# Kernel tuning notes

Hardware: AMD Instinct MI355X
Metric: run time of the kernel (lower is better)

## Reference

```python
import jax, jax.numpy as jnp
import numpy as np

B, S, D, H, FF = 8, 1024, 2048, 16, 8192
Dh = D // H
EPS = 1e-5

def _layernorm(x, g, b):
    m = jnp.mean(x, axis=-1, keepdims=True)
    v = jnp.mean(jnp.square(x - m), axis=-1, keepdims=True)
    return (x - m) / jnp.sqrt(v + EPS) * g + b

def setup_inputs() -> dict:
    key = jax.random.key(0)
    ks = jax.random.split(key, 12)
    sc_d = 1.0 / np.sqrt(D)
    sc_ff = 1.0 / np.sqrt(FF)
    return {
        "x": jax.random.normal(ks[0], (B, S, D), dtype=jnp.float32),
        "mask": jnp.ones((S, S), dtype=jnp.int32),
        "Wq": jax.random.normal(ks[1], (D, D), dtype=jnp.float32) * sc_d,
        "bq": jnp.zeros((D,), dtype=jnp.float32),
        "Wk": jax.random.normal(ks[2], (D, D), dtype=jnp.float32) * sc_d,
        "bk": jnp.zeros((D,), dtype=jnp.float32),
        "Wv": jax.random.normal(ks[3], (D, D), dtype=jnp.float32) * sc_d,
        "bv": jnp.zeros((D,), dtype=jnp.float32),
        "Wo": jax.random.normal(ks[4], (D, D), dtype=jnp.float32) * sc_d,
        "bo": jnp.zeros((D,), dtype=jnp.float32),
        "W1": jax.random.normal(ks[5], (FF, D), dtype=jnp.float32) * sc_d,
        "b1": jnp.zeros((FF,), dtype=jnp.float32),
        "W2": jax.random.normal(ks[6], (D, FF), dtype=jnp.float32) * sc_ff,
        "b2": jnp.zeros((D,), dtype=jnp.float32),
        "g1": jnp.ones((D,), dtype=jnp.float32),
        "be1": jnp.zeros((D,), dtype=jnp.float32),
        "g2": jnp.ones((D,), dtype=jnp.float32),
        "be2": jnp.zeros((D,), dtype=jnp.float32),
    }

def reference(x, mask, Wq, bq, Wk, bk, Wv, bv, Wo, bo, W1, b1, W2, b2, g1, be1, g2, be2):
    # --- multi-head attention (chunk along d_model == reshape to heads) ---
    q = (x @ Wq.T + bq).reshape(B, S, H, Dh)
    k = (x @ Wk.T + bk).reshape(B, S, H, Dh)
    v = (x @ Wv.T + bv).reshape(B, S, H, Dh)
    score = jnp.einsum('bqhd,bkhd->bhqk', q, k) / jnp.sqrt(jnp.float32(Dh))
    score = jnp.where(mask == 0, jnp.float32(-1e9), score)
    attn = jax.nn.softmax(score, axis=-1)
    out = jnp.einsum('bhqk,bkhd->bqhd', attn, v).reshape(B, S, D)
    attn_out = out @ Wo.T + bo
    # --- residual + post-LN ---
    x1 = _layernorm(attn_out + x, g1, be1)
    # --- FFN ---
    h = jax.nn.relu(x1 @ W1.T + b1)
    ffn_out = h @ W2.T + b2
    return _layernorm(ffn_out + x1, g2, be2)
```

## Files before the change

kernel.cpp:

```cpp
#include <hip/hip_runtime.h>
#include <cstdint>
#include <cstddef>


typedef unsigned short u16;
typedef unsigned int   u32;
typedef unsigned long long u64;
typedef __attribute__((ext_vector_type(8))) short short8;
typedef __attribute__((ext_vector_type(4))) float f32x4;

constexpr int Bc  = 8;
constexpr int Sc  = 1024;
constexpr int Dc  = 2048;
constexpr int Hc  = 16;
constexpr int Dhc = 128;
constexpr int FFc = 8192;
constexpr int Mc  = Bc * Sc;

__device__ __forceinline__ u16 f2b(float f) {
  u32 u = __builtin_bit_cast(u32, f);
  u += 0x7fffu + ((u >> 16) & 1u);
  return (u16)(u >> 16);
}
__device__ __forceinline__ u32 pack2(float a, float b) {
  return (u32)f2b(a) | ((u32)f2b(b) << 16);
}
__device__ __forceinline__ void unpack8(uint4 u, float* f) {
  u32 w[4] = {u.x, u.y, u.z, u.w};
#pragma unroll
  for (int i = 0; i < 4; ++i) {
    f[2 * i + 0] = __builtin_bit_cast(float, w[i] << 16);
    f[2 * i + 1] = __builtin_bit_cast(float, w[i] & 0xffff0000u);
  }
}

#define GLOAD_LDS16(gp, lp)                                                    \
  __builtin_amdgcn_global_load_lds(                                            \
      (const __attribute__((address_space(1))) void*)(gp),                     \
      (__attribute__((address_space(3))) void*)(lp), 16, 0, 0)

__global__ __launch_bounds__(256) void cvt_f32_bf16(const float* __restrict__ in,
                                                    u16* __restrict__ out, int n) {
  int i = (blockIdx.x * 256 + threadIdx.x) << 2;
  if (i >= n) return;
  float4 v = *(const float4*)(in + i);
  ushort4 o;
  o.x = f2b(v.x); o.y = f2b(v.y); o.z = f2b(v.z); o.w = f2b(v.w);
  *(ushort4*)(out + i) = o;
}

__global__ __launch_bounds__(256) void mask_bits(const int* __restrict__ mask,
                                                 u64* __restrict__ mb) {
  int t = blockIdx.x * 256 + threadIdx.x;
  int r = t >> 4, wd = t & 15;
  const int* p = mask + (size_t)r * Sc + wd * 64;
  u64 bits = 0;
#pragma unroll 16
  for (int i = 0; i < 64; i += 4) {
    int4 q = *(const int4*)(p + i);
    bits |= (u64)(q.x != 0) << (i + 0);
    bits |= (u64)(q.y != 0) << (i + 1);
    bits |= (u64)(q.z != 0) << (i + 2);
    bits |= (u64)(q.w != 0) << (i + 3);
  }
  mb[t] = bits;
}

template <int MODE>
__global__ __launch_bounds__(512, 2) void gemm256tb(const u16* __restrict__ A,
                                                    const u16* __restrict__ Bt,
                                                    const float* __restrict__ bias,
                                                    u16* __restrict__ C,
                                                    int M, int N, int K) {
  __shared__ u16 Abuf[4][256 * 32];
  __shared__ u16 Bbuf[4][256 * 32];

  const int nbn = N >> 8;
  const int nwg = (M >> 8) * nbn;
  int bid = blockIdx.x;
  int sw = (bid & 7) * (nwg >> 3) + (bid >> 3);
  const int m0 = (sw / nbn) << 8;
  const int n0 = (sw % nbn) << 8;

  const int tid  = threadIdx.x;
  const int lane = tid & 63;
  const int w    = tid >> 6;
  const int wm   = w >> 2;
  const int wn   = w & 3;

  const int rowA = lane & 15;
  const int g4   = lane >> 4;

  const int p16  = lane << 4;
  const int wsw  = p16 ^ (((p16 >> 9) & 1) << 5);
  const int s_rr = wsw >> 6;
  const int s_cc = (wsw & 63) >> 1;

  const int sb = (rowA * 64 + g4 * 16) ^ (((rowA >> 3) & 1) << 5);

  const int NT = K >> 5;

  const u16* Asrc = A  + (size_t)(m0 + w * 32 + s_rr) * K + s_cc;
  const u16* Bsrc = Bt + (size_t)(n0 + w * 32 + s_rr) * K + s_cc;

  auto stageA = [&](int buf, int tt) {
#pragma unroll
    for (int i = 0; i < 2; ++i)
      GLOAD_LDS16(Asrc + (size_t)i * 16 * K + tt * 32,
                  &Abuf[buf][(2 * w + i) * 512]);
  };
  auto stageB = [&](int buf, int tt) {
#pragma unroll
    for (int i = 0; i < 2; ++i)
      GLOAD_LDS16(Bsrc + (size_t)i * 16 * K + tt * 32,
                  &Bbuf[buf][(2 * w + i) * 512]);
  };

  f32x4 acc[8][4];
#pragma unroll
  for (int m = 0; m < 8; ++m)
#pragma unroll
    for (int n = 0; n < 4; ++n) acc[m][n] = (f32x4){0.f, 0.f, 0.f, 0.f};

  stageA(0, 0); stageB(0, 0);
  stageA(1, 1); stageB(1, 1);
  stageA(2, 2); stageB(2, 2);
  asm volatile("s_waitcnt vmcnt(8)" ::: "memory");
  __builtin_amdgcn_s_barrier();

  for (int t = 0; t < NT; ++t) {
    const int rd  = t & 3;
    const int wr_ = (t + 3) & 3;
    const bool st = (t + 3) < NT;

    short8 bF[4], aF[4];
#pragma unroll
    for (int n = 0; n < 4; ++n)
      bF[n] = *(const short8*)((const char*)&Bbuf[rd][(wn * 4 + n) * 512] + sb);
#pragma unroll
    for (int i = 0; i < 4; ++i)
      aF[i] = *(const short8*)((const char*)&Abuf[rd][(wm * 8 + i) * 512] + sb);
    if (st) stageA(wr_, t + 3);
    __builtin_amdgcn_s_barrier();
    asm volatile("s_waitcnt lgkmcnt(0)" ::: "memory");
    __builtin_amdgcn_sched_barrier(0);
    __builtin_amdgcn_s_setprio(1);
#pragma unroll
    for (int i = 0; i < 4; ++i)
#pragma unroll
      for (int n = 0; n < 4; ++n)
        acc[i][n] = __builtin_amdgcn_mfma_f32_16x16x32_bf16(aF[i], bF[n], acc[i][n], 0, 0, 0);
    __builtin_amdgcn_s_setprio(0);
    __builtin_amdgcn_s_barrier();

#pragma unroll
    for (int i = 0; i < 4; ++i)
      aF[i] = *(const short8*)((const char*)&Abuf[rd][(wm * 8 + 4 + i) * 512] + sb);
    if (st) stageB(wr_, t + 3);
    __builtin_amdgcn_s_barrier();
    asm volatile("s_waitcnt lgkmcnt(0)" ::: "memory");
    __builtin_amdgcn_sched_barrier(0);
    __builtin_amdgcn_s_setprio(1);
#pragma unroll
    for (int i = 0; i < 4; ++i)
#pragma unroll
      for (int n = 0; n < 4; ++n)
        acc[4 + i][n] = __builtin_amdgcn_mfma_f32_16x16x32_bf16(aF[i], bF[n], acc[4 + i][n], 0, 0, 0);
    __builtin_amdgcn_s_setprio(0);
    if (st)                { asm volatile("s_waitcnt vmcnt(8)" ::: "memory"); }
    else if (t + 2 < NT)   { asm volatile("s_waitcnt vmcnt(4)" ::: "memory"); }
    else                   { asm volatile("s_waitcnt vmcnt(0)" ::: "memory"); }
    __builtin_amdgcn_s_barrier();
  }

  const int ci = lane & 15;
  const int ri = g4 << 2;
  float bvv[4];
#pragma unroll
  for (int n = 0; n < 4; ++n) bvv[n] = bias[n0 + wn * 64 + n * 16 + ci];

  if (MODE == 2) {
#pragma unroll
    for (int n = 0; n < 4; ++n) {
      int col = n0 + wn * 64 + n * 16 + ci;
#pragma unroll
      for (int m = 0; m < 8; ++m) {
        int row0 = m0 + wm * 128 + m * 16 + ri;
        ushort4 pk;
        pk.x = f2b(acc[m][n][0] + bvv[n]);
        pk.y = f2b(acc[m][n][1] + bvv[n]);
        pk.z = f2b(acc[m][n][2] + bvv[n]);
        pk.w = f2b(acc[m][n][3] + bvv[n]);
        size_t addr = ((size_t)((row0 >> 10) * Hc + (col >> 7)) * 128 + (col & 127)) * 1024
                      + (row0 & 1023);
        *(ushort4*)(C + addr) = pk;
      }
    }
  } else {
#pragma unroll
    for (int m = 0; m < 8; ++m) {
      int row0 = m0 + wm * 128 + m * 16 + ri;
#pragma unroll
      for (int j = 0; j < 4; ++j) {
        u16* cp = C + (size_t)(row0 + j) * N + n0 + wn * 64 + ci;
#pragma unroll
        for (int n = 0; n < 4; ++n) {
          float v = acc[m][n][j] + bvv[n];
          if (MODE == 1) v = fmaxf(v, 0.f);
          cp[n * 16] = f2b(v);
        }
      }
    }
  }
}

__global__ __launch_bounds__(256, 2) void attn_mfma(
    const u16* __restrict__ qb,
    const u16* __restrict__ kb,
    const u16* __restrict__ vt,
    const u64* __restrict__ mb,
    u16* __restrict__ ob)
{
  __shared__ u16 Ks[64 * 128];
  __shared__ u16 Vts[128 * 64];
  __shared__ u16 Ps[4][32 * 64];

  const int bid = blockIdx.x;
  const int l   = (bid & 7) * 128 + (bid >> 3);
  const int qt  = l & 7;
  const int bh  = l >> 3;
  const int h   = bh & (Hc - 1);
  const int b   = bh >> 4;
  const int q0  = qt * 128;

  const int tid  = threadIdx.x;
  const int lane = tid & 63;
  const int w    = tid >> 6;
  const int rowA = lane & 15;
  const int g4   = lane >> 4;
  const int kq16 = g4 << 3;
  const int ri   = g4 << 2;

  const size_t tokbase = (size_t)b * Sc * Dc + (size_t)h * Dhc;
  const size_t vtbase  = (size_t)bh * 128 * 1024;
  const int qwbase = q0 + w * 32;

  short8 qf[2][4];
#pragma unroll
  for (int m = 0; m < 2; ++m)
#pragma unroll
    for (int kk = 0; kk < 4; ++kk)
      qf[m][kk] = *reinterpret_cast<const short8*>(
          qb + tokbase + (size_t)(qwbase + m * 16 + rowA) * Dc + kk * 32 + kq16);

  f32x4 O[2][8];
#pragma unroll
  for (int m = 0; m < 2; ++m)
#pragma unroll
    for (int n = 0; n < 8; ++n) O[m][n] = (f32x4){0.f, 0.f, 0.f, 0.f};
  float mrow[2][4], lrow[2][4];
#pragma unroll
  for (int m = 0; m < 2; ++m)
#pragma unroll
    for (int j = 0; j < 4; ++j) { mrow[m][j] = -INFINITY; lrow[m][j] = 0.f; }

  const float scale = 0.08838834764831845f;

  for (int kt = 0; kt < Sc / 64; ++kt) {
    const int k0 = kt * 64;
    __syncthreads();
#pragma unroll
    for (int i = 0; i < 4; ++i) {
      int chunk = w * 4 + i;
      int gb = (chunk * 64 + lane) * 16;
      int L  = gb ^ (((gb >> 8) & 7) << 4);
      int row = L >> 8, ce = (L & 255) >> 1;
      GLOAD_LDS16(kb + tokbase + (size_t)(k0 + row) * Dc + ce, &Ks[chunk * 512]);
    }
#pragma unroll
    for (int i = 0; i < 4; ++i) {
      int chunk = w * 4 + i;
      int gb = (chunk * 64 + lane) * 16;
      int L  = gb ^ (((gb >> 7) & 7) << 4);
      int row = L >> 7, ce = (L & 127) >> 1;
      GLOAD_LDS16(vt + vtbase + (size_t)row * 1024 + k0 + ce, &Vts[chunk * 512]);
    }
    __syncthreads();

    f32x4 s[2][4];
#pragma unroll
    for (int m = 0; m < 2; ++m)
#pragma unroll
      for (int n = 0; n < 4; ++n) s[m][n] = (f32x4){0.f, 0.f, 0.f, 0.f};
#pragma unroll
    for (int kk = 0; kk < 4; ++kk) {
      short8 bfk[4];
#pragma unroll
      for (int n = 0; n < 4; ++n) {
        int krow = n * 16 + rowA;
        int by = (krow * 256 + kk * 64 + (g4 << 4)) ^ ((krow & 7) << 4);
        bfk[n] = *reinterpret_cast<const short8*>((const char*)Ks + by);
      }
#pragma unroll
      for (int m = 0; m < 2; ++m)
#pragma unroll
        for (int n = 0; n < 4; ++n)
          s[m][n] = __builtin_amdgcn_mfma_f32_16x16x32_bf16(qf[m][kk], bfk[n], s[m][n], 0, 0, 0);
    }

    float alpha[2][4];
#pragma unroll
    for (int m = 0; m < 2; ++m) {
      u64 wb_[4];
#pragma unroll
      for (int j = 0; j < 4; ++j)
        wb_[j] = mb[(size_t)(qwbase + m * 16 + ri + j) * 16 + kt];
#pragma unroll
      for (int j = 0; j < 4; ++j) {
        float pv[4];
        float mx = -3.0e38f;
#pragma unroll
        for (int n = 0; n < 4; ++n) {
          float x = s[m][n][j] * scale;
          if (!((wb_[j] >> (n * 16 + rowA)) & 1)) x = -1e9f;
          pv[n] = x;
          mx = fmaxf(mx, x);
        }
        mx = fmaxf(mx, __shfl_xor(mx, 1));
        mx = fmaxf(mx, __shfl_xor(mx, 2));
        mx = fmaxf(mx, __shfl_xor(mx, 4));
        mx = fmaxf(mx, __shfl_xor(mx, 8));
        float mnew = fmaxf(mrow[m][j], mx);
        float a = __expf(mrow[m][j] - mnew);
        mrow[m][j] = mnew;
        alpha[m][j] = a;
        float rs = 0.f;
#pragma unroll
        for (int n = 0; n < 4; ++n) {
          float p = __expf(pv[n] - mnew);
          pv[n] = p;
          rs += p;
        }
        rs += __shfl_xor(rs, 1);
        rs += __shfl_xor(rs, 2);
        rs += __shfl_xor(rs, 4);
        rs += __shfl_xor(rs, 8);
        lrow[m][j] = lrow[m][j] * a + rs;
        int prow = m * 16 + ri + j;
#pragma unroll
        for (int n = 0; n < 4; ++n) {
          int by = (prow * 128 + 2 * (n * 16 + rowA)) ^ ((prow & 7) << 4);
          *(u16*)((char*)Ps[w] + by) = f2b(pv[n]);
        }
      }
    }
    asm volatile("s_waitcnt lgkmcnt(0)" ::: "memory");

#pragma unroll
    for (int m = 0; m < 2; ++m)
#pragma unroll
      for (int n = 0; n < 8; ++n)
#pragma unroll
        for (int j = 0; j < 4; ++j) O[m][n][j] *= alpha[m][j];

    short8 pa[2][2];
#pragma unroll
    for (int m = 0; m < 2; ++m)
#pragma unroll
      for (int kk = 0; kk < 2; ++kk) {
        int prow = m * 16 + rowA;
        int by = (prow * 128 + kk * 64 + (g4 << 4)) ^ ((prow & 7) << 4);
        pa[m][kk] = *reinterpret_cast<const short8*>((const char*)Ps[w] + by);
      }
#pragma unroll
    for (int kk = 0; kk < 2; ++kk)
#pragma unroll
      for (int n = 0; n < 8; ++n) {
        int drow = n * 16 + rowA;
        int by = (drow * 128 + kk * 64 + (g4 << 4)) ^ ((drow & 7) << 4);
        short8 bfv = *reinterpret_cast<const short8*>((const char*)Vts + by);
#pragma unroll
        for (int m = 0; m < 2; ++m)
          O[m][n] = __builtin_amdgcn_mfma_f32_16x16x32_bf16(pa[m][kk], bfv, O[m][n], 0, 0, 0);
      }
  }

  float inv[2][4];
#pragma unroll
  for (int m = 0; m < 2; ++m)
#pragma unroll
    for (int j = 0; j < 4; ++j) inv[m][j] = 1.f / lrow[m][j];
#pragma unroll
  for (int m = 0; m < 2; ++m)
#pragma unroll
    for (int n = 0; n < 8; ++n) {
      int dcol = n * 16 + rowA;
#pragma unroll
      for (int j = 0; j < 4; ++j) {
        int qg = qwbase + m * 16 + ri + j;
        ob[tokbase + (size_t)qg * Dc + dcol] = f2b(O[m][n][j] * inv[m][j]);
      }
    }
}

template <int RES_BF16, int OUT_BF16>
__global__ __launch_bounds__(256) void ln_kernel(const u16* __restrict__ a,
                                                 const void* __restrict__ resid,
                                                 const float* __restrict__ g,
                                                 const float* __restrict__ be,
                                                 void* __restrict__ out) {
  int row = blockIdx.x;
  int tid = threadIdx.x;
  int c0  = tid << 3;

  float v[8], vr[8];
  uint4 ua = *(const uint4*)(a + (size_t)row * Dc + c0);
  unpack8(ua, v);
  if (RES_BF16) {
    uint4 ur = *(const uint4*)((const u16*)resid + (size_t)row * Dc + c0);
    unpack8(ur, vr);
  } else {
    const float* rp = (const float*)resid + (size_t)row * Dc + c0;
    float4 f0 = *(const float4*)rp;
    float4 f1 = *(const float4*)(rp + 4);
    vr[0] = f0.x; vr[1] = f0.y; vr[2] = f0.z; vr[3] = f0.w;
    vr[4] = f1.x; vr[5] = f1.y; vr[6] = f1.z; vr[7] = f1.w;
  }

  float s = 0.f, ss = 0.f;
#pragma unroll
  for (int j = 0; j < 8; ++j) {
    v[j] += vr[j];
    s += v[j];
    ss += v[j] * v[j];
  }
#pragma unroll
  for (int off = 32; off; off >>= 1) {
    s  += __shfl_down(s, off);
    ss += __shfl_down(ss, off);
  }
  __shared__ float rs[4], rss[4], stat[2];
  if ((tid & 63) == 0) { rs[tid >> 6] = s; rss[tid >> 6] = ss; }
  __syncthreads();
  if (tid == 0) {
    float t  = rs[0] + rs[1] + rs[2] + rs[3];
    float tt = rss[0] + rss[1] + rss[2] + rss[3];
    float mean = t * (1.f / Dc);
    float var  = tt * (1.f / Dc) - mean * mean;
    stat[0] = mean;
    stat[1] = rsqrtf(var + 1e-5f);
  }
  __syncthreads();
  float mean = stat[0], rstd = stat[1];

  float y[8];
#pragma unroll
  for (int j = 0; j < 8; ++j) y[j] = (v[j] - mean) * rstd * g[c0 + j] + be[c0 + j];

  if (OUT_BF16) {
    uint4 o;
    o.x = pack2(y[0], y[1]); o.y = pack2(y[2], y[3]);
    o.z = pack2(y[4], y[5]); o.w = pack2(y[6], y[7]);
    *(uint4*)((u16*)out + (size_t)row * Dc + c0) = o;
  } else {
    float* op = (float*)out + (size_t)row * Dc + c0;
    *(float4*)op       = (float4){y[0], y[1], y[2], y[3]};
    *(float4*)(op + 4) = (float4){y[4], y[5], y[6], y[7]};
  }
}

extern "C" void kernel_launch(void* const* d_in, const int* in_sizes, int n_in,
                              void* d_out, int out_size, void* d_ws, size_t ws_size,
                              hipStream_t stream) {
  (void)in_sizes; (void)n_in; (void)out_size; (void)ws_size;

  const float* x   = (const float*)d_in[0];
  const int*   mk  = (const int*)d_in[1];
  const float* Wq  = (const float*)d_in[2];
  const float* bq  = (const float*)d_in[3];
  const float* Wk  = (const float*)d_in[4];
  const float* bk  = (const float*)d_in[5];
  const float* Wv  = (const float*)d_in[6];
  const float* bv  = (const float*)d_in[7];
  const float* Wo  = (const float*)d_in[8];
  const float* bo  = (const float*)d_in[9];
  const float* W1  = (const float*)d_in[10];
  const float* b1  = (const float*)d_in[11];
  const float* W2  = (const float*)d_in[12];
  const float* b2  = (const float*)d_in[13];
  const float* g1  = (const float*)d_in[14];
  const float* be1 = (const float*)d_in[15];
  const float* g2  = (const float*)d_in[16];
  const float* be2 = (const float*)d_in[17];
  float* outp = (float*)d_out;

  const size_t R = 16777216;
  u16* xb  = (u16*)d_ws;
  u16* wb  = xb + R;
  u16* qb  = wb + R;
  u16* kb  = qb + R;
  u16* vt  = kb + R;
  u16* ao  = vt + R;
  u64* mbt = (u64*)d_ws;
  u16* ap  = qb;
  u16* x1  = kb;
  u16* hb  = vt;
  u16* ffn = xb;

  auto cvt = [&](const float* src, u16* dst, int n) {
    cvt_f32_bf16<<<dim3((n + 1023) / 1024), dim3(256), 0, stream>>>(src, dst, n);
  };

  cvt(x, xb, Mc * Dc);

  cvt(Wq, wb, Dc * Dc);
  gemm256tb<0><<<dim3(32 * 8), dim3(512), 0, stream>>>(xb, wb, bq, qb, Mc, Dc, Dc);
  cvt(Wk, wb, Dc * Dc);
  gemm256tb<0><<<dim3(32 * 8), dim3(512), 0, stream>>>(xb, wb, bk, kb, Mc, Dc, Dc);
  cvt(Wv, wb, Dc * Dc);
  gemm256tb<2><<<dim3(32 * 8), dim3(512), 0, stream>>>(xb, wb, bv, vt, Mc, Dc, Dc);

  mask_bits<<<dim3(64), dim3(256), 0, stream>>>(mk, mbt);

  attn_mfma<<<dim3(Bc * Hc * (Sc / 128)), dim3(256), 0, stream>>>(qb, kb, vt, mbt, ao);

  cvt(Wo, wb, Dc * Dc);
  gemm256tb<0><<<dim3(32 * 8), dim3(512), 0, stream>>>(ao, wb, bo, ap, Mc, Dc, Dc);
  ln_kernel<0, 1><<<dim3(Mc), dim3(256), 0, stream>>>(ap, x, g1, be1, x1);

  cvt(W1, wb, FFc * Dc);
  gemm256tb<1><<<dim3(32 * 32), dim3(512), 0, stream>>>(x1, wb, b1, hb, Mc, FFc, Dc);
  cvt(W2, wb, Dc * FFc);
  gemm256tb<0><<<dim3(32 * 8), dim3(512), 0, stream>>>(hb, wb, b2, ffn, Mc, Dc, FFc);
  ln_kernel<1, 0><<<dim3(Mc), dim3(256), 0, stream>>>(ffn, x1, g2, be2, outp);
}
```

Before: 1.155 ms.

## Double-buffer MFMA fragments in registers and cut per-tile barriers

```diff
diff --git a/kernel.cpp b/kernel.cpp
--- a/kernel.cpp
+++ b/kernel.cpp
@@ -103,17 +103,24 @@
   const u16* Asrc = A  + (size_t)(m0 + w * 32 + s_rr) * K + s_cc;
   const u16* Bsrc = Bt + (size_t)(n0 + w * 32 + s_rr) * K + s_cc;
 
-  auto stageA = [&](int buf, int tt) {
+  auto stage = [&](int tt) {
+    int buf = tt & 3;
 #pragma unroll
     for (int i = 0; i < 2; ++i)
-      GLOAD_LDS16(Asrc + (size_t)i * 16 * K + tt * 32,
-                  &Abuf[buf][(2 * w + i) * 512]);
+      GLOAD_LDS16(Asrc + (size_t)i * 16 * K + tt * 32, &Abuf[buf][(2 * w + i) * 512]);
+#pragma unroll
+    for (int i = 0; i < 2; ++i)
+      GLOAD_LDS16(Bsrc + (size_t)i * 16 * K + tt * 32, &Bbuf[buf][(2 * w + i) * 512]);
   };
-  auto stageB = [&](int buf, int tt) {
-#pragma unroll
-    for (int i = 0; i < 2; ++i)
-      GLOAD_LDS16(Bsrc + (size_t)i * 16 * K + tt * 32,
-                  &Bbuf[buf][(2 * w + i) * 512]);
+
+  auto readF = [&](int tt, short8* aF, short8* bF) {
+    int buf = tt & 3;
+#pragma unroll
+    for (int n = 0; n < 4; ++n)
+      bF[n] = *(const short8*)((const char*)&Bbuf[buf][(wn * 4 + n) * 512] + sb);
+#pragma unroll
+    for (int i = 0; i < 8; ++i)
+      aF[i] = *(const short8*)((const char*)&Abuf[buf][(wm * 8 + i) * 512] + sb);
   };
 
   f32x4 acc[8][4];
@@ -122,55 +129,32 @@
 #pragma unroll
     for (int n = 0; n < 4; ++n) acc[m][n] = (f32x4){0.f, 0.f, 0.f, 0.f};
 
-  stageA(0, 0); stageB(0, 0);
-  stageA(1, 1); stageB(1, 1);
-  stageA(2, 2); stageB(2, 2);
-  asm volatile("s_waitcnt vmcnt(8)" ::: "memory");
+  stage(0); stage(1); stage(2);
+  asm volatile("s_waitcnt vmcnt(4)" ::: "memory");
   __builtin_amdgcn_s_barrier();
 
-  for (int t = 0; t < NT; ++t) {
-    const int rd  = t & 3;
-    const int wr_ = (t + 3) & 3;
-    const bool st = (t + 3) < NT;
-
-    short8 bF[4], aF[4];
-#pragma unroll
-    for (int n = 0; n < 4; ++n)
-      bF[n] = *(const short8*)((const char*)&Bbuf[rd][(wn * 4 + n) * 512] + sb);
-#pragma unroll
-    for (int i = 0; i < 4; ++i)
-      aF[i] = *(const short8*)((const char*)&Abuf[rd][(wm * 8 + i) * 512] + sb);
-    if (st) stageA(wr_, t + 3);
-    __builtin_amdgcn_s_barrier();
-    asm volatile("s_waitcnt lgkmcnt(0)" ::: "memory");
+  short8 a0[8], b0[4], a1[8], b1[4];
+  readF(0, a0, b0);
+
+  auto body = [&](int t, short8* aC, short8* bC, short8* aN, short8* bN) {
+    if (t + 1 < NT) readF(t + 1, aN, bN);
+    if (t + 3 < NT) stage(t + 3);
     __builtin_amdgcn_sched_barrier(0);
     __builtin_amdgcn_s_setprio(1);
 #pragma unroll
-    for (int i = 0; i < 4; ++i)
+    for (int i = 0; i < 8; ++i)
 #pragma unroll
       for (int n = 0; n < 4; ++n)
-        acc[i][n] = __builtin_amdgcn_mfma_f32_16x16x32_bf16(aF[i], bF[n], acc[i][n], 0, 0, 0);
+        acc[i][n] = __builtin_amdgcn_mfma_f32_16x16x32_bf16(aC[i], bC[n], acc[i][n], 0, 0, 0);
     __builtin_amdgcn_s_setprio(0);
+    if (t + 3 < NT) { asm volatile("s_waitcnt vmcnt(4)" ::: "memory"); }
+    else            { asm volatile("s_waitcnt vmcnt(0)" ::: "memory"); }
     __builtin_amdgcn_s_barrier();
-
-#pragma unroll
-    for (int i = 0; i < 4; ++i)
-      aF[i] = *(const short8*)((const char*)&Abuf[rd][(wm * 8 + 4 + i) * 512] + sb);
-    if (st) stageB(wr_, t + 3);
-    __builtin_amdgcn_s_barrier();
-    asm volatile("s_waitcnt lgkmcnt(0)" ::: "memory");
-    __builtin_amdgcn_sched_barrier(0);
-    __builtin_amdgcn_s_setprio(1);
-#pragma unroll
-    for (int i = 0; i < 4; ++i)
-#pragma unroll
-      for (int n = 0; n < 4; ++n)
-        acc[4 + i][n] = __builtin_amdgcn_mfma_f32_16x16x32_bf16(aF[i], bF[n], acc[4 + i][n], 0, 0, 0);
-    __builtin_amdgcn_s_setprio(0);
-    if (st)                { asm volatile("s_waitcnt vmcnt(8)" ::: "memory"); }
-    else if (t + 2 < NT)   { asm volatile("s_waitcnt vmcnt(4)" ::: "memory"); }
-    else                   { asm volatile("s_waitcnt vmcnt(0)" ::: "memory"); }
-    __builtin_amdgcn_s_barrier();
+  };
+
+  for (int t = 0; t < NT; t += 2) {
+    body(t,     a0, b0, a1, b1);
+    body(t + 1, a1, b1, a0, b0);
   }
 
   const int ci = lane & 15;
```

After: 1.046 ms. -9.4%, faster.
